# Kernel tuning notes

Measured on AMD Instinct MI355X. Metric: run time of the kernel, lower is better.

The kernel has to match this reference:

```python
import jax, jax.numpy as jnp
import numpy as np

N, D_IN, D_OUT = 4096, 1024, 1024
DROPOUT_RATE = 0.1


def setup_inputs() -> dict:
    key = jax.random.key(0)
    kx, kq, kk, kv = jax.random.split(key, 4)
    s = 1.0 / np.sqrt(D_IN)
    return {
        "x": jax.random.normal(kx, (N, D_IN), dtype=jnp.float32),
        "wq": jax.random.normal(kq, (D_OUT, D_IN), dtype=jnp.float32) * s,
        "wk": jax.random.normal(kk, (D_OUT, D_IN), dtype=jnp.float32) * s,
        "wv": jax.random.normal(kv, (D_OUT, D_IN), dtype=jnp.float32) * s,
    }


def reference(x, wq, wk, wv):
    # torch Linear: y = x @ W.T  (no bias since qkv_bias=False)
    q = x @ wq.T                      # [N, d_out]
    k = x @ wk.T
    v = x @ wv.T
    scores = q @ k.T                  # [N, N]
    n = scores.shape[0]
    causal = jnp.tril(jnp.ones((n, n), dtype=bool))  # keep lower triangle
    masked = jnp.where(causal, scores, -jnp.inf)
    scale = k.shape[-1] ** 0.5
    weights = jax.nn.softmax(masked / scale, axis=-1)
    # dropout (train mode), fixed key for determinism
    keep = jax.random.bernoulli(jax.random.key(42), 1.0 - DROPOUT_RATE, weights.shape)
    weights = jnp.where(keep, weights / (1.0 - DROPOUT_RATE), 0.0)
    return weights @ v                # [N, d_out]
```

## Files before the change

### kernel.cpp

```cpp
#include <hip/hip_runtime.h>
#include <hip/hip_fp16.h>

typedef __attribute__((ext_vector_type(8))) _Float16 f16x8;
typedef __attribute__((ext_vector_type(4))) float f32x4;

typedef const __attribute__((address_space(1))) void gas_void;
typedef __attribute__((address_space(3))) void las_void;
typedef __attribute__((address_space(3))) const __half las_chalf;

__device__ __forceinline__ f16x8 ldsr(const __half* p) {
    f16x8 r;
    asm volatile("ds_read_b128 %0, %1" : "=v"(r) : "v"((las_chalf*)p));
    return r;
}

__global__ __launch_bounds__(256) void cast_f32_f16_k(const float* __restrict__ in,
                                                      __half* __restrict__ out, int n) {
    int i = (blockIdx.x * 256 + threadIdx.x) * 8;
    if (i >= n) return;
    float4 a = *(const float4*)(in + i);
    float4 b = *(const float4*)(in + i + 4);
    __half2 h[4] = { __floats2half2_rn(a.x, a.y), __floats2half2_rn(a.z, a.w),
                     __floats2half2_rn(b.x, b.y), __floats2half2_rn(b.z, b.w) };
    *(int4*)(out + i) = *(int4*)h;
}

__global__ __launch_bounds__(256) void transpose_f16_k(const __half* __restrict__ in,
                                                       __half* __restrict__ out,
                                                       int R, int ldin) {
    __shared__ __half t[64][72];
    int r0 = blockIdx.x * 64, c0 = blockIdx.y * 64;
    for (int idx = threadIdx.x; idx < 64 * 64; idx += 256) {
        int r = idx >> 6, c = idx & 63;
        t[r][c] = in[(size_t)(r0 + r) * ldin + c0 + c];
    }
    __syncthreads();
    for (int idx = threadIdx.x; idx < 64 * 64; idx += 256) {
        int r = idx >> 6, c = idx & 63;
        out[(size_t)(c0 + r) * R + r0 + c] = t[c][r];
    }
}

__device__ __forceinline__ void storeC(__half* C, size_t off, float v) { C[off] = __float2half(v); }
__device__ __forceinline__ void storeC(float*  C, size_t off, float v) { C[off] = v; }

template <typename CT, bool LOWER_ONLY>
__global__ __launch_bounds__(512, 2)
void gemm256(const __half* __restrict__ A, const __half* __restrict__ B, CT* __restrict__ C,
             int lda, int ldb, int ldc, int NT, float scale) {
    const int bi = blockIdx.x, bj = blockIdx.y;
    if (LOWER_ONLY && bj > bi) return;
    const int brow = bi * 256, bcol = bj * 256;
    const int tid = threadIdx.x;
    const int lane = tid & 63, wid = tid >> 6;
    const int wm = wid >> 2, wn = wid & 3;
    const int lane15 = lane & 15;
    const int kxor = (lane & 7) << 3;
    const int g16 = (lane >> 4) << 3;

    extern __shared__ __half smem[];

    const int srow = (wid << 3) + (lane >> 3);
    const int scol = ((lane & 7) ^ ((lane >> 3) & 7)) << 3;

    auto stage_half = [&](const __half* G, int ldg, int growbase, int kt, int buf, int mat, int half) {
        const __half* src = G + (size_t)(growbase + half * 128 + srow) * ldg + kt * 64 + scol;
        __half* dst = &smem[buf * 32768 + mat * 16384 + (half * 128 + (wid << 3)) * 64];
        __builtin_amdgcn_global_load_lds((gas_void*)src, (las_void*)dst, 16, 0, 0);
        __builtin_amdgcn_global_load_lds((gas_void*)(src + (size_t)64 * ldg),
                                         (las_void*)(dst + 64 * 64), 16, 0, 0);
    };

    f32x4 acc[8][4] = {};
    f16x8 bfrag[2][4];

    stage_half(B, ldb, bcol, 0, 0, 1, 0);
    stage_half(B, ldb, bcol, 0, 0, 1, 1);
    stage_half(A, lda, brow, 0, 0, 0, 0);
    stage_half(A, lda, brow, 0, 0, 0, 1);
    if (NT > 1) {
        stage_half(B, ldb, bcol, 1, 1, 1, 0);
        stage_half(B, ldb, bcol, 1, 1, 1, 1);
    }

    for (int T = 0; T < NT; ++T) {
        const int buf = T & 1;
        const __half* Abase = &smem[buf * 32768 + (wm * 128 + lane15) * 64];
        const __half* Bbase = &smem[buf * 32768 + 16384 + (wn * 64 + lane15) * 64];

        if (T < NT - 1) asm volatile("s_waitcnt vmcnt(4)" ::: "memory");
        else            asm volatile("s_waitcnt vmcnt(0)" ::: "memory");
        __builtin_amdgcn_s_barrier();

        {
#pragma unroll
            for (int kk = 0; kk < 2; ++kk)
#pragma unroll
                for (int n = 0; n < 4; ++n)
                    bfrag[kk][n] = ldsr(Bbase + (n * 16) * 64 + ((kk * 32 + g16) ^ kxor));
            f16x8 af[2][2];
#pragma unroll
            for (int mi = 0; mi < 2; ++mi)
#pragma unroll
                for (int kk = 0; kk < 2; ++kk)
                    af[mi][kk] = ldsr(Abase + (mi * 16) * 64 + ((kk * 32 + g16) ^ kxor));
            if (T + 1 < NT) stage_half(A, lda, brow, T + 1, (T + 1) & 1, 0, 0);
            asm volatile("s_waitcnt lgkmcnt(0)" ::: "memory");
            __builtin_amdgcn_sched_barrier(0);
            __builtin_amdgcn_s_setprio(1);
#pragma unroll
            for (int mi = 0; mi < 2; ++mi)
#pragma unroll
                for (int n = 0; n < 4; ++n)
#pragma unroll
                    for (int kk = 0; kk < 2; ++kk)
                        acc[mi][n] = __builtin_amdgcn_mfma_f32_16x16x32_f16(
                            af[mi][kk], bfrag[kk][n], acc[mi][n], 0, 0, 0);
            __builtin_amdgcn_s_setprio(0);
            __builtin_amdgcn_s_barrier();
        }

#pragma unroll
        for (int p = 1; p < 4; ++p) {
            f16x8 af[2][2];
#pragma unroll
            for (int mi = 0; mi < 2; ++mi)
#pragma unroll
                for (int kk = 0; kk < 2; ++kk)
                    af[mi][kk] = ldsr(Abase + ((2 * p + mi) * 16) * 64 + ((kk * 32 + g16) ^ kxor));
            if (p == 1)      { if (T + 1 < NT) stage_half(A, lda, brow, T + 1, (T + 1) & 1, 0, 1); }
            else if (p == 2) { if (T + 2 < NT) stage_half(B, ldb, bcol, T + 2, T & 1, 1, 0); }
            else             { if (T + 2 < NT) stage_half(B, ldb, bcol, T + 2, T & 1, 1, 1); }
            asm volatile("s_waitcnt lgkmcnt(0)" ::: "memory");
            __builtin_amdgcn_sched_barrier(0);
            __builtin_amdgcn_s_setprio(1);
#pragma unroll
            for (int mi = 0; mi < 2; ++mi)
#pragma unroll
                for (int n = 0; n < 4; ++n)
#pragma unroll
                    for (int kk = 0; kk < 2; ++kk)
                        acc[2 * p + mi][n] = __builtin_amdgcn_mfma_f32_16x16x32_f16(
                            af[mi][kk], bfrag[kk][n], acc[2 * p + mi][n], 0, 0, 0);
            __builtin_amdgcn_s_setprio(0);
            __builtin_amdgcn_s_barrier();
        }
    }

    const int r0 = (lane >> 4) << 2;
#pragma unroll
    for (int m = 0; m < 8; ++m) {
#pragma unroll
        for (int n = 0; n < 4; ++n) {
            int col = bcol + wn * 64 + n * 16 + lane15;
#pragma unroll
            for (int r = 0; r < 4; ++r) {
                int row = brow + wm * 128 + m * 16 + r0 + r;
                storeC(C, (size_t)row * ldc + col, acc[m][n][r] * scale);
            }
        }
    }
}

__device__ __forceinline__ void stage_tile(const __half* Ag, const __half* Bg, int lda, int ldb,
                                           __half* As, __half* Bs, int wid, int k0) {
#pragma unroll
    for (int it = 0; it < 4; ++it) {
        __builtin_amdgcn_global_load_lds(
            (gas_void*)(Ag + (size_t)it * 8 * lda + k0),
            (las_void*)(&As[((wid << 5) + it * 8) * 64]), 16, 0, 0);
        __builtin_amdgcn_global_load_lds(
            (gas_void*)(Bg + (size_t)it * 8 * ldb + k0),
            (las_void*)(&Bs[((wid << 5) + it * 8) * 64]), 16, 0, 0);
    }
}

__global__ __launch_bounds__(256)
void gemm_pv(const __half* __restrict__ A, const __half* __restrict__ B, float* __restrict__ C,
             float* __restrict__ P1, float* __restrict__ P2, float* __restrict__ P3,
             int lda, int ldb, int ldc) {
    int bi, c;
    const int bj = blockIdx.y;
    {
        int x = blockIdx.x;
        if (x < 8)       { bi = x;                    c = 0; }
        else if (x < 24) { bi = 8  + ((x - 8) >> 1);  c = (x - 8) & 1; }
        else if (x < 48) { bi = 16 + (x - 24) / 3;    c = (x - 24) % 3; }
        else             { bi = 24 + ((x - 48) >> 2); c = (x - 48) & 3; }
    }
    const int brow = bi * 128, bcol = bj * 128;
    const int tid = threadIdx.x, lane = tid & 63, wid = tid >> 6;
    const int wr = (wid >> 1) * 64, wc = (wid & 1) * 64;

    const int full = 2 * (bi + 1);
    const int k_lo = c * 16, k_hi = min(full, k_lo + 16);

    __shared__ __align__(16) __half As[2][128 * 64];
    __shared__ __align__(16) __half Bs[2][128 * 64];

    f32x4 acc[4][4] = {};

    const int srow = (wid << 5) + (lane >> 3);
    const int skc  = (lane & 7) << 3;
    const __half* Ag = A + (size_t)(brow + srow) * lda + skc;
    const __half* Bg = B + (size_t)(bcol + srow) * ldb + skc;

    int cur = 0;
    stage_tile(Ag, Bg, lda, ldb, As[0], Bs[0], wid, k_lo << 6);
    __syncthreads();

    for (int kt = k_lo; kt < k_hi; ++kt) {
        if (kt + 1 < k_hi)
            stage_tile(Ag, Bg, lda, ldb, As[cur ^ 1], Bs[cur ^ 1], wid, (kt + 1) << 6);
        const __half* Asb = As[cur];
        const __half* Bsb = Bs[cur];
#pragma unroll
        for (int kk = 0; kk < 2; ++kk) {
            const int ko = kk * 32 + ((lane >> 4) << 3);
            f16x8 af[4], bf[4];
#pragma unroll
            for (int m = 0; m < 4; ++m)
                af[m] = *(const f16x8*)(&Asb[(wr + m * 16 + (lane & 15)) * 64 + ko]);
#pragma unroll
            for (int n = 0; n < 4; ++n)
                bf[n] = *(const f16x8*)(&Bsb[(wc + n * 16 + (lane & 15)) * 64 + ko]);
#pragma unroll
            for (int m = 0; m < 4; ++m)
#pragma unroll
                for (int n = 0; n < 4; ++n)
                    acc[m][n] = __builtin_amdgcn_mfma_f32_16x16x32_f16(af[m], bf[n], acc[m][n], 0, 0, 0);
        }
        __syncthreads();
        cur ^= 1;
    }

    float* Ct = C;
    if (c == 1) Ct = P1; else if (c == 2) Ct = P2; else if (c == 3) Ct = P3;

    const int r0 = (lane >> 4) << 2;
    const int cc = lane & 15;
#pragma unroll
    for (int m = 0; m < 4; ++m) {
#pragma unroll
        for (int n = 0; n < 4; ++n) {
            int col = bcol + wc + n * 16 + cc;
#pragma unroll
            for (int r = 0; r < 4; ++r) {
                int row = brow + wr + m * 16 + r0 + r;
                Ct[(size_t)row * ldc + col] = acc[m][n][r];
            }
        }
    }
}

__global__ __launch_bounds__(256) void pv_reduce_k(float* __restrict__ out,
                                                   const float* __restrict__ P1,
                                                   const float* __restrict__ P2,
                                                   const float* __restrict__ P3) {
    const int row = 1024 + blockIdx.x;
    const size_t o = (size_t)row * 1024 + threadIdx.x * 4;
    float4 s = *(float4*)(out + o);
    float4 a = *(const float4*)(P1 + o);
    s.x += a.x; s.y += a.y; s.z += a.z; s.w += a.w;
    if (row >= 2048) {
        float4 b = *(const float4*)(P2 + o);
        s.x += b.x; s.y += b.y; s.z += b.z; s.w += b.w;
    }
    if (row >= 3072) {
        float4 d = *(const float4*)(P3 + o);
        s.x += d.x; s.y += d.y; s.z += d.z; s.w += d.w;
    }
    *(float4*)(out + o) = s;
}

__device__ __forceinline__ uint32_t rotl32(uint32_t x, int d) { return (x << d) | (x >> (32 - d)); }

__device__ __forceinline__ bool keep_bit(uint32_t i, uint32_t j) {
    uint32_t x0 = 0u;
    uint32_t x1 = i * 4096u + j;
    const uint32_t ks0 = 0u, ks1 = 42u, ks2 = 0u ^ 42u ^ 0x1BD11BDAu;
    x0 += ks0; x1 += ks1;
#define TFR(r) { x0 += x1; x1 = rotl32(x1, r); x1 ^= x0; }
    TFR(13) TFR(15) TFR(26) TFR(6)   x0 += ks1; x1 += ks2 + 1u;
    TFR(17) TFR(29) TFR(16) TFR(24)  x0 += ks2; x1 += ks0 + 2u;
    TFR(13) TFR(15) TFR(26) TFR(6)   x0 += ks0; x1 += ks1 + 3u;
    TFR(17) TFR(29) TFR(16) TFR(24)  x0 += ks1; x1 += ks2 + 4u;
    TFR(13) TFR(15) TFR(26) TFR(6)   x0 += ks2; x1 += ks0 + 5u;
#undef TFR
    uint32_t bits = x0 ^ x1;
    float u = __uint_as_float((bits >> 9) | 0x3f800000u) - 1.0f;
    return u < 0.9f;
}

__global__ __launch_bounds__(256) void softmax_dropout_k(__half* __restrict__ SP, int N) {
    const int i = blockIdx.x;
    const int tid = threadIdx.x;
    const int len = i + 1;
    __half* row = SP + (size_t)i * N;

    float m = -1.0e30f, l = 0.f;
    const int len8 = len & ~7;
    for (int j = tid * 8; j < len8; j += 2048) {
        int4 pk = *(const int4*)(row + j);
        const __half2* h2 = (const __half2*)&pk;
#pragma unroll
        for (int q = 0; q < 4; ++q) {
            float2 f2 = __half22float2(h2[q]);
            float nm = fmaxf(m, fmaxf(f2.x, f2.y));
            l = l * __expf(m - nm) + __expf(f2.x - nm) + __expf(f2.y - nm);
            m = nm;
        }
    }
    for (int j = len8 + tid; j < len; j += 256) {
        float s = __half2float(row[j]);
        float nm = fmaxf(m, s);
        l = l * __expf(m - nm) + __expf(s - nm);
        m = nm;
    }
    for (int off = 1; off < 64; off <<= 1) {
        float m2 = __shfl_xor(m, off);
        float l2 = __shfl_xor(l, off);
        float nm = fmaxf(m, m2);
        l = l * __expf(m - nm) + l2 * __expf(m2 - nm);
        m = nm;
    }
    __shared__ float ms[4], ls[4];
    if ((tid & 63) == 0) { ms[tid >> 6] = m; ls[tid >> 6] = l; }
    __syncthreads();
    float M = ms[0], L = ls[0];
#pragma unroll
    for (int w = 1; w < 4; ++w) {
        float nm = fmaxf(M, ms[w]);
        L = L * __expf(M - nm) + ls[w] * __expf(ms[w] - nm);
        M = nm;
    }
    const float inv = 1.0f / (L * 0.9f);

    for (int j = tid; j < len; j += 256) {
        float s = __half2float(row[j]);
        float w = __expf(s - M) * inv;
        row[j] = keep_bit((uint32_t)i, (uint32_t)j) ? __float2half(w) : __float2half(0.0f);
    }
    const int zlim = ((i >> 7) << 7) + 128;
    for (int j = len + tid; j < zlim; j += 256) row[j] = __float2half(0.0f);
}

extern "C" void kernel_launch(void* const* d_in, const int* in_sizes, int n_in,
                              void* d_out, int out_size, void* d_ws, size_t ws_size,
                              hipStream_t stream) {
    const float* x  = (const float*)d_in[0];
    const float* wq = (const float*)d_in[1];
    const float* wk = (const float*)d_in[2];
    const float* wv = (const float*)d_in[3];
    float* out = (float*)d_out;
    char* ws = (char*)d_ws;

    const int N = 4096, D = 1024;

    __half* xb   = (__half*)(ws + 0);
    __half* wqkv = (__half*)(ws + 8388608);
    __half* QKV  = (__half*)(ws + 14680064);
    __half* VT   = (__half*)(ws + 39845888);
    __half* SP   = (__half*)(ws + 48234496);

    float* P1 = (float*)(ws + 14680064) - (size_t)1024 * 1024;
    float* P2 = (float*)(ws + 14680064 + 12582912) - (size_t)2048 * 1024;
    float* P3 = (float*)(ws + 14680064 + 20971520) - (size_t)3072 * 1024;

    __half* Q = QKV;
    __half* K = QKV + 1024;
    __half* V = QKV + 2048;

    auto* gqkv_f = gemm256<__half, false>;
    auto* gs_f   = gemm256<__half, true>;
    (void)hipFuncSetAttribute((const void*)gqkv_f, hipFuncAttributeMaxDynamicSharedMemorySize, 131072);
    (void)hipFuncSetAttribute((const void*)gs_f,   hipFuncAttributeMaxDynamicSharedMemorySize, 131072);

    cast_f32_f16_k<<<2048, 256, 0, stream>>>(x,  xb,  N * D);
    cast_f32_f16_k<<<512,  256, 0, stream>>>(wq, wqkv,             D * D);
    cast_f32_f16_k<<<512,  256, 0, stream>>>(wk, wqkv + D * D,     D * D);
    cast_f32_f16_k<<<512,  256, 0, stream>>>(wv, wqkv + 2 * D * D, D * D);

    dim3 gq(N / 256, 3 * D / 256);
    gqkv_f<<<gq, 512, 131072, stream>>>(xb, wqkv, QKV, D, D, 3 * D, D / 64, 1.0f);

    dim3 gt(N / 64, D / 64);
    transpose_f16_k<<<gt, 256, 0, stream>>>(V, VT, N, 3 * D);

    dim3 gsd(N / 256, N / 256);
    gs_f<<<gsd, 512, 131072, stream>>>(Q, K, SP, 3 * D, 3 * D, N, D / 64, 0.03125f);

    softmax_dropout_k<<<N, 256, 0, stream>>>(SP, N);

    dim3 go(80, D / 128);
    gemm_pv<<<go, 256, 0, stream>>>(SP, VT, out, P1, P2, P3, N, N, D);
    pv_reduce_k<<<3072, 256, 0, stream>>>(out, P1, P2, P3);
}
```

Before: 172.0 us.

## Run PV matmul through the 256-tile pipelined GEMM with causal split-K

Replaces the separate 128x128 PV GEMM with a split-K mode of the 256x256 pipelined gemm256 kernel. Row blocks map to 1–4 K-chunks of 16 tiles each, limited by the causal extent, and the partials go to the same P1/P2/P3 buffers. Softmax zero-fill now runs to the 256-aligned boundary so the larger tiles read zeros past the diagonal. The three weight casts are also merged into one launch. The aim is to get more MFMA work per LDS read and a better-pipelined mainloop for PV, at the cost of coarser causal granularity and only 160 blocks.

```diff
diff --git a/kernel.cpp b/kernel.cpp
--- a/kernel.cpp
+++ b/kernel.cpp
@@ -25,6 +25,20 @@
     *(int4*)(out + i) = *(int4*)h;
 }
 
+__global__ __launch_bounds__(256) void cast3_f32_f16_k(const float* __restrict__ a,
+                                                       const float* __restrict__ b,
+                                                       const float* __restrict__ c,
+                                                       __half* __restrict__ out) {
+    const int which = blockIdx.x >> 9;
+    const float* src = which == 0 ? a : (which == 1 ? b : c);
+    const int i = (((blockIdx.x & 511) * 256) + threadIdx.x) * 8;
+    float4 va = *(const float4*)(src + i);
+    float4 vb = *(const float4*)(src + i + 4);
+    __half2 h[4] = { __floats2half2_rn(va.x, va.y), __floats2half2_rn(va.z, va.w),
+                     __floats2half2_rn(vb.x, vb.y), __floats2half2_rn(vb.z, vb.w) };
+    *(int4*)(out + (size_t)which * 1048576 + i) = *(int4*)h;
+}
+
 __global__ __launch_bounds__(256) void transpose_f16_k(const __half* __restrict__ in,
                                                        __half* __restrict__ out,
                                                        int R, int ldin) {
@@ -44,12 +58,23 @@
 __device__ __forceinline__ void storeC(__half* C, size_t off, float v) { C[off] = __float2half(v); }
 __device__ __forceinline__ void storeC(float*  C, size_t off, float v) { C[off] = v; }
 
-template <typename CT, bool LOWER_ONLY>
+template <typename CT, bool LOWER_ONLY, bool SPLITK>
 __global__ __launch_bounds__(512, 2)
 void gemm256(const __half* __restrict__ A, const __half* __restrict__ B, CT* __restrict__ C,
-             int lda, int ldb, int ldc, int NT, float scale) {
-    const int bi = blockIdx.x, bj = blockIdx.y;
-    if (LOWER_ONLY && bj > bi) return;
+             float* __restrict__ P1, float* __restrict__ P2, float* __restrict__ P3,
+             int lda, int ldb, int ldc, int NTin, float scale) {
+    int bi, c = 0;
+    const int bj = blockIdx.y;
+    if (SPLITK) {
+        int x = blockIdx.x;
+        if (x < 4)       { bi = x;                    c = 0; }
+        else if (x < 12) { bi = 4  + ((x - 4) >> 1);  c = (x - 4) & 1; }
+        else if (x < 24) { bi = 8  + (x - 12) / 3;    c = (x - 12) % 3; }
+        else             { bi = 12 + ((x - 24) >> 2); c = (x - 24) & 3; }
+    } else {
+        bi = blockIdx.x;
+        if (LOWER_ONLY && bj > bi) return;
+    }
     const int brow = bi * 256, bcol = bj * 256;
     const int tid = threadIdx.x;
     const int lane = tid & 63, wid = tid >> 6;
@@ -58,6 +83,9 @@
     const int kxor = (lane & 7) << 3;
     const int g16 = (lane >> 4) << 3;
 
+    int k_lo = 0, NT = NTin;
+    if (SPLITK) { int full = 4 * (bi + 1); k_lo = c * 16; NT = min(full - k_lo, 16); }
+
     extern __shared__ __half smem[];
 
     const int srow = (wid << 3) + (lane >> 3);
@@ -74,22 +102,23 @@
     f32x4 acc[8][4] = {};
     f16x8 bfrag[2][4];
 
-    stage_half(B, ldb, bcol, 0, 0, 1, 0);
-    stage_half(B, ldb, bcol, 0, 0, 1, 1);
-    stage_half(A, lda, brow, 0, 0, 0, 0);
-    stage_half(A, lda, brow, 0, 0, 0, 1);
+    stage_half(B, ldb, bcol, k_lo, 0, 1, 0);
+    stage_half(B, ldb, bcol, k_lo, 0, 1, 1);
+    stage_half(A, lda, brow, k_lo, 0, 0, 0);
+    stage_half(A, lda, brow, k_lo, 0, 0, 1);
     if (NT > 1) {
-        stage_half(B, ldb, bcol, 1, 1, 1, 0);
-        stage_half(B, ldb, bcol, 1, 1, 1, 1);
-    }
-
-    for (int T = 0; T < NT; ++T) {
-        const int buf = T & 1;
+        stage_half(B, ldb, bcol, k_lo + 1, 1, 1, 0);
+        stage_half(B, ldb, bcol, k_lo + 1, 1, 1, 1);
+    }
+
+    for (int Tr = 0; Tr < NT; ++Tr) {
+        const int Ta = k_lo + Tr;
+        const int buf = Tr & 1;
         const __half* Abase = &smem[buf * 32768 + (wm * 128 + lane15) * 64];
         const __half* Bbase = &smem[buf * 32768 + 16384 + (wn * 64 + lane15) * 64];
 
-        if (T < NT - 1) asm volatile("s_waitcnt vmcnt(4)" ::: "memory");
-        else            asm volatile("s_waitcnt vmcnt(0)" ::: "memory");
+        if (Tr < NT - 1) asm volatile("s_waitcnt vmcnt(4)" ::: "memory");
+        else             asm volatile("s_waitcnt vmcnt(0)" ::: "memory");
         __builtin_amdgcn_s_barrier();
 
         {
@@ -104,7 +133,7 @@
 #pragma unroll
                 for (int kk = 0; kk < 2; ++kk)
                     af[mi][kk] = ldsr(Abase + (mi * 16) * 64 + ((kk * 32 + g16) ^ kxor));
-            if (T + 1 < NT) stage_half(A, lda, brow, T + 1, (T + 1) & 1, 0, 0);
+            if (Tr + 1 < NT) stage_half(A, lda, brow, Ta + 1, buf ^ 1, 0, 0);
             asm volatile("s_waitcnt lgkmcnt(0)" ::: "memory");
             __builtin_amdgcn_sched_barrier(0);
             __builtin_amdgcn_s_setprio(1);
@@ -128,9 +157,9 @@
 #pragma unroll
                 for (int kk = 0; kk < 2; ++kk)
                     af[mi][kk] = ldsr(Abase + ((2 * p + mi) * 16) * 64 + ((kk * 32 + g16) ^ kxor));
-            if (p == 1)      { if (T + 1 < NT) stage_half(A, lda, brow, T + 1, (T + 1) & 1, 0, 1); }
-            else if (p == 2) { if (T + 2 < NT) stage_half(B, ldb, bcol, T + 2, T & 1, 1, 0); }
-            else             { if (T + 2 < NT) stage_half(B, ldb, bcol, T + 2, T & 1, 1, 1); }
+            if (p == 1)      { if (Tr + 1 < NT) stage_half(A, lda, brow, Ta + 1, buf ^ 1, 0, 1); }
+            else if (p == 2) { if (Tr + 2 < NT) stage_half(B, ldb, bcol, Ta + 2, buf, 1, 0); }
+            else             { if (Tr + 2 < NT) stage_half(B, ldb, bcol, Ta + 2, buf, 1, 1); }
             asm volatile("s_waitcnt lgkmcnt(0)" ::: "memory");
             __builtin_amdgcn_sched_barrier(0);
             __builtin_amdgcn_s_setprio(1);
@@ -147,6 +176,8 @@
         }
     }
 
+    CT* Ct = C;
+    if (SPLITK && c > 0) Ct = (CT*)(c == 1 ? P1 : (c == 2 ? P2 : P3));
     const int r0 = (lane >> 4) << 2;
 #pragma unroll
     for (int m = 0; m < 8; ++m) {
@@ -156,98 +187,7 @@
 #pragma unroll
             for (int r = 0; r < 4; ++r) {
                 int row = brow + wm * 128 + m * 16 + r0 + r;
-                storeC(C, (size_t)row * ldc + col, acc[m][n][r] * scale);
-            }
-        }
-    }
-}
-
-__device__ __forceinline__ void stage_tile(const __half* Ag, const __half* Bg, int lda, int ldb,
-                                           __half* As, __half* Bs, int wid, int k0) {
-#pragma unroll
-    for (int it = 0; it < 4; ++it) {
-        __builtin_amdgcn_global_load_lds(
-            (gas_void*)(Ag + (size_t)it * 8 * lda + k0),
-            (las_void*)(&As[((wid << 5) + it * 8) * 64]), 16, 0, 0);
-        __builtin_amdgcn_global_load_lds(
-            (gas_void*)(Bg + (size_t)it * 8 * ldb + k0),
-            (las_void*)(&Bs[((wid << 5) + it * 8) * 64]), 16, 0, 0);
-    }
-}
-
-__global__ __launch_bounds__(256)
-void gemm_pv(const __half* __restrict__ A, const __half* __restrict__ B, float* __restrict__ C,
-             float* __restrict__ P1, float* __restrict__ P2, float* __restrict__ P3,
-             int lda, int ldb, int ldc) {
-    int bi, c;
-    const int bj = blockIdx.y;
-    {
-        int x = blockIdx.x;
-        if (x < 8)       { bi = x;                    c = 0; }
-        else if (x < 24) { bi = 8  + ((x - 8) >> 1);  c = (x - 8) & 1; }
-        else if (x < 48) { bi = 16 + (x - 24) / 3;    c = (x - 24) % 3; }
-        else             { bi = 24 + ((x - 48) >> 2); c = (x - 48) & 3; }
-    }
-    const int brow = bi * 128, bcol = bj * 128;
-    const int tid = threadIdx.x, lane = tid & 63, wid = tid >> 6;
-    const int wr = (wid >> 1) * 64, wc = (wid & 1) * 64;
-
-    const int full = 2 * (bi + 1);
-    const int k_lo = c * 16, k_hi = min(full, k_lo + 16);
-
-    __shared__ __align__(16) __half As[2][128 * 64];
-    __shared__ __align__(16) __half Bs[2][128 * 64];
-
-    f32x4 acc[4][4] = {};
-
-    const int srow = (wid << 5) + (lane >> 3);
-    const int skc  = (lane & 7) << 3;
-    const __half* Ag = A + (size_t)(brow + srow) * lda + skc;
-    const __half* Bg = B + (size_t)(bcol + srow) * ldb + skc;
-
-    int cur = 0;
-    stage_tile(Ag, Bg, lda, ldb, As[0], Bs[0], wid, k_lo << 6);
-    __syncthreads();
-
-    for (int kt = k_lo; kt < k_hi; ++kt) {
-        if (kt + 1 < k_hi)
-            stage_tile(Ag, Bg, lda, ldb, As[cur ^ 1], Bs[cur ^ 1], wid, (kt + 1) << 6);
-        const __half* Asb = As[cur];
-        const __half* Bsb = Bs[cur];
-#pragma unroll
-        for (int kk = 0; kk < 2; ++kk) {
-            const int ko = kk * 32 + ((lane >> 4) << 3);
-            f16x8 af[4], bf[4];
-#pragma unroll
-            for (int m = 0; m < 4; ++m)
-                af[m] = *(const f16x8*)(&Asb[(wr + m * 16 + (lane & 15)) * 64 + ko]);
-#pragma unroll
-            for (int n = 0; n < 4; ++n)
-                bf[n] = *(const f16x8*)(&Bsb[(wc + n * 16 + (lane & 15)) * 64 + ko]);
-#pragma unroll
-            for (int m = 0; m < 4; ++m)
-#pragma unroll
-                for (int n = 0; n < 4; ++n)
-                    acc[m][n] = __builtin_amdgcn_mfma_f32_16x16x32_f16(af[m], bf[n], acc[m][n], 0, 0, 0);
-        }
-        __syncthreads();
-        cur ^= 1;
-    }
-
-    float* Ct = C;
-    if (c == 1) Ct = P1; else if (c == 2) Ct = P2; else if (c == 3) Ct = P3;
-
-    const int r0 = (lane >> 4) << 2;
-    const int cc = lane & 15;
-#pragma unroll
-    for (int m = 0; m < 4; ++m) {
-#pragma unroll
-        for (int n = 0; n < 4; ++n) {
-            int col = bcol + wc + n * 16 + cc;
-#pragma unroll
-            for (int r = 0; r < 4; ++r) {
-                int row = brow + wr + m * 16 + r0 + r;
-                Ct[(size_t)row * ldc + col] = acc[m][n][r];
+                storeC(Ct, (size_t)row * ldc + col, acc[m][n][r] * scale);
             }
         }
     }
@@ -341,7 +281,7 @@
         float w = __expf(s - M) * inv;
         row[j] = keep_bit((uint32_t)i, (uint32_t)j) ? __float2half(w) : __float2half(0.0f);
     }
-    const int zlim = ((i >> 7) << 7) + 128;
+    const int zlim = ((i >> 8) << 8) + 256;
     for (int j = len + tid; j < zlim; j += 256) row[j] = __float2half(0.0f);
 }
 
@@ -371,28 +311,31 @@
     __half* K = QKV + 1024;
     __half* V = QKV + 2048;
 
-    auto* gqkv_f = gemm256<__half, false>;
-    auto* gs_f   = gemm256<__half, true>;
+    auto* gqkv_f = gemm256<__half, false, false>;
+    auto* gs_f   = gemm256<__half, true,  false>;
+    auto* gpv_f  = gemm256<float,  false, true>;
     (void)hipFuncSetAttribute((const void*)gqkv_f, hipFuncAttributeMaxDynamicSharedMemorySize, 131072);
     (void)hipFuncSetAttribute((const void*)gs_f,   hipFuncAttributeMaxDynamicSharedMemorySize, 131072);
-
-    cast_f32_f16_k<<<2048, 256, 0, stream>>>(x,  xb,  N * D);
-    cast_f32_f16_k<<<512,  256, 0, stream>>>(wq, wqkv,             D * D);
-    cast_f32_f16_k<<<512,  256, 0, stream>>>(wk, wqkv + D * D,     D * D);
-    cast_f32_f16_k<<<512,  256, 0, stream>>>(wv, wqkv + 2 * D * D, D * D);
+    (void)hipFuncSetAttribute((const void*)gpv_f,  hipFuncAttributeMaxDynamicSharedMemorySize, 131072);
+
+    cast_f32_f16_k<<<2048, 256, 0, stream>>>(x, xb, N * D);
+    cast3_f32_f16_k<<<1536, 256, 0, stream>>>(wq, wk, wv, wqkv);
 
     dim3 gq(N / 256, 3 * D / 256);
-    gqkv_f<<<gq, 512, 131072, stream>>>(xb, wqkv, QKV, D, D, 3 * D, D / 64, 1.0f);
+    gqkv_f<<<gq, 512, 131072, stream>>>(xb, wqkv, QKV, nullptr, nullptr, nullptr,
+                                        D, D, 3 * D, D / 64, 1.0f);
 
     dim3 gt(N / 64, D / 64);
     transpose_f16_k<<<gt, 256, 0, stream>>>(V, VT, N, 3 * D);
 
     dim3 gsd(N / 256, N / 256);
-    gs_f<<<gsd, 512, 131072, stream>>>(Q, K, SP, 3 * D, 3 * D, N, D / 64, 0.03125f);
+    gs_f<<<gsd, 512, 131072, stream>>>(Q, K, SP, nullptr, nullptr, nullptr,
+                                       3 * D, 3 * D, N, D / 64, 0.03125f);
 
     softmax_dropout_k<<<N, 256, 0, stream>>>(SP, N);
 
-    dim3 go(80, D / 128);
-    gemm_pv<<<go, 256, 0, stream>>>(SP, VT, out, P1, P2, P3, N, N, D);
+    dim3 go(40, D / 256);
+    gpv_f<<<go, 512, 131072, stream>>>(SP, VT, out, P1, P2, P3,
+                                       N, N, D, 0, 1.0f);
     pv_reduce_k<<<3072, 256, 0, stream>>>(out, P1, P2, P3);
 }
```

New measurement: 154.5 us. -10.2%, faster.
